# Kernel tuning notes

Measured on AMD Instinct MI355X. Metric: run time of the kernel, lower is better.

## Reference

```python
import jax, jax.numpy as jnp
import numpy as np

COMMITMENT_COST = 0.25
NUM_EMBEDDINGS = 512
EMBEDDING_DIM = 64


def setup_inputs() -> dict:
    key = jax.random.key(0)
    k1, k2 = jax.random.split(key)
    inputs = jax.random.normal(k1, (32, EMBEDDING_DIM, 64, 64), dtype=jnp.float32)  # NCHW
    embedding_weight = jax.random.normal(k2, (NUM_EMBEDDINGS, EMBEDDING_DIM), dtype=jnp.float32)
    return {"inputs": inputs, "embedding_weight": embedding_weight}


def reference(inputs, embedding_weight):
    # NCHW -> NHWC, flatten to [N, D]
    x = jnp.transpose(inputs, (0, 2, 3, 1))  # [B,H,W,D]
    input_shape = x.shape
    flat = x.reshape(-1, EMBEDDING_DIM)  # [N, D]

    distances = (jnp.sum(flat * flat, axis=1, keepdims=True)
                 + jnp.sum(embedding_weight * embedding_weight, axis=1)
                 - 2.0 * jnp.matmul(flat, embedding_weight.T))

    encoding_indices = jnp.argmin(distances, axis=1)  # [N]
    encodings = jax.nn.one_hot(encoding_indices, NUM_EMBEDDINGS, dtype=jnp.float32)  # [N, K]

    # quantized lookup (== encodings @ embedding_weight)
    quantized = jnp.take(embedding_weight, encoding_indices, axis=0).reshape(input_shape)

    # commitment loss (eval path; EMA buffer updates are a training-time side effect)
    encoder_loss = jnp.mean((jax.lax.stop_gradient(quantized) - x) ** 2)
    loss = COMMITMENT_COST * encoder_loss

    # straight-through estimator
    quantized_st = x + jax.lax.stop_gradient(quantized - x)

    avg_probs = jnp.mean(encodings, axis=0)
    perplexity = jnp.exp(-jnp.sum(avg_probs * jnp.log(avg_probs + 1e-10)))

    return (loss, jnp.transpose(quantized_st, (0, 3, 1, 2)), perplexity, encodings)
```

## Files before the change

### kernel.cpp

```cpp
#include <hip/hip_runtime.h>
#include <math.h>

#define N_ROWS 131072
#define D 64
#define K 512
#define BLK 512
#define ROWS_PER_BLK 512
#define GRID (N_ROWS / ROWS_PER_BLK)
#define MARGIN 4e-3f


typedef __attribute__((ext_vector_type(8))) _Float16 f16x8;
typedef __attribute__((ext_vector_type(4))) float    f32x4;

#define MFMA(a, b, c) __builtin_amdgcn_mfma_f32_16x16x32_f16((a), (b), (c), 0, 0, 0)

#define OFF_EH   0
#define OFF_EL   65536
#define OFF_XH   0
#define OFF_XL   65536
#define OFF_E2   131072
#define OFF_IDX  133120
#define OFF_REF  135168
#define ARENA_SZ 137216

__global__ __launch_bounds__(256) void vq_e2_kernel(
    const float* __restrict__ emb, float* __restrict__ e2)
{
    int k = blockIdx.x * blockDim.x + threadIdx.x;
    if (k < K) {
        const float* e = emb + k * D;
        float s = 0.f;
        #pragma unroll
        for (int d = 0; d < D; ++d) s = fmaf(e[d], e[d], s);
        e2[k] = s;
    }
}

__device__ __forceinline__ unsigned pk2(_Float16 a, _Float16 b) {
    return (unsigned)__builtin_bit_cast(unsigned short, a) |
           ((unsigned)__builtin_bit_cast(unsigned short, b) << 16);
}

#define CT_ALL(M) M(0) M(1) M(2) M(3)
#define UPD(rt, s, ki) { \
    bool lt1 = (s) < s1_##rt; bool lt2 = (s) < s2_##rt; \
    s2_##rt = lt1 ? s1_##rt : (lt2 ? (s) : s2_##rt); \
    i2_##rt = lt1 ? i1_##rt : (lt2 ? (ki) : i2_##rt); \
    s1_##rt = lt1 ? (s) : s1_##rt; \
    i1_##rt = lt1 ? (ki) : i1_##rt; }

__device__ __forceinline__ void dist_pass(
    const char* ebase, const float* e2L, int fq, int fr,
    f16x8 xh0_0, f16x8 xh0_1, f16x8 xl0_0, f16x8 xl0_1,
    f16x8 xh1_0, f16x8 xh1_1, f16x8 xl1_0, f16x8 xl1_1,
    int* s_idxL, int* s_refL, int row0)
{
    float s1_0 = INFINITY, s2_0 = INFINITY, s1_1 = INFINITY, s2_1 = INFINITY;
    int   i1_0 = 0, i2_0 = 0, i1_1 = 0, i2_1 = 0;

    for (int cb = 0; cb < 8; ++cb) {
        const int cbBase = cb * 64 + fq * 4;

#define LDE2(ct) f32x4 e2q##ct = *(const f32x4*)(e2L + cb * 64 + ct * 16 + fq * 4);
        CT_ALL(LDE2)
#undef LDE2

#define LDE(ct) \
        const int c##ct = cb * 64 + ct * 16 + fr; \
        const char* rb##ct = ebase + c##ct * 128; \
        const unsigned xr##ct = (unsigned)((c##ct & 7) << 4); \
        f16x8 eh##ct##_0 = *(const f16x8*)(rb##ct + OFF_EH + (((unsigned)(fq*16 +  0)) ^ xr##ct)); \
        f16x8 eh##ct##_1 = *(const f16x8*)(rb##ct + OFF_EH + (((unsigned)(fq*16 + 64)) ^ xr##ct)); \
        f16x8 el##ct##_0 = *(const f16x8*)(rb##ct + OFF_EL + (((unsigned)(fq*16 +  0)) ^ xr##ct)); \
        f16x8 el##ct##_1 = *(const f16x8*)(rb##ct + OFF_EL + (((unsigned)(fq*16 + 64)) ^ xr##ct));
        CT_ALL(LDE)
#undef LDE

#define ACC1(rt, ct) \
        f32x4 a##rt##_##ct = {0.f, 0.f, 0.f, 0.f}; \
        a##rt##_##ct = MFMA(eh##ct##_0, xh##rt##_0, a##rt##_##ct); \
        a##rt##_##ct = MFMA(eh##ct##_1, xh##rt##_1, a##rt##_##ct); \
        a##rt##_##ct = MFMA(el##ct##_0, xh##rt##_0, a##rt##_##ct); \
        a##rt##_##ct = MFMA(el##ct##_1, xh##rt##_1, a##rt##_##ct); \
        a##rt##_##ct = MFMA(eh##ct##_0, xl##rt##_0, a##rt##_##ct); \
        a##rt##_##ct = MFMA(eh##ct##_1, xl##rt##_1, a##rt##_##ct);
#define ACC_CT(ct) ACC1(0, ct) ACC1(1, ct)
        CT_ALL(ACC_CT)
#undef ACC_CT
#undef ACC1

#define SCJ(rt, ct, j) { \
        float s = fmaf(-2.f, a##rt##_##ct[j], e2q##ct[j]); \
        int ki = cbBase + ct * 16 + j; \
        UPD(rt, s, ki) }
#define SC4(rt, ct) SCJ(rt, ct, 0) SCJ(rt, ct, 1) SCJ(rt, ct, 2) SCJ(rt, ct, 3)
#define SC_CT(ct) SC4(0, ct) SC4(1, ct)
        CT_ALL(SC_CT)
#undef SC_CT
#undef SC4
#undef SCJ
    }

#define MERGE(rt, off) { \
    float b1 = __shfl_xor(s1_##rt, off); int bi1 = __shfl_xor(i1_##rt, off); \
    float b2 = __shfl_xor(s2_##rt, off); int bi2 = __shfl_xor(i2_##rt, off); \
    bool bf = (b1 < s1_##rt) || (b1 == s1_##rt && bi1 < i1_##rt); \
    float c1 = bf ? b1 : s1_##rt; int ci1 = bf ? bi1 : i1_##rt; \
    float lw = bf ? s1_##rt : b1; int lwi = bf ? i1_##rt : bi1; \
    float d2 = bf ? b2 : s2_##rt; int di2 = bf ? bi2 : i2_##rt; \
    bool ds = (d2 < lw) || (d2 == lw && di2 < lwi); \
    s1_##rt = c1; i1_##rt = ci1; \
    s2_##rt = ds ? d2 : lw; i2_##rt = ds ? di2 : lwi; }
    MERGE(0, 16) MERGE(0, 32) MERGE(1, 16) MERGE(1, 32)
#undef MERGE

    if (fq == 0) {
        s_idxL[row0 + fr] = i1_0;
        s_refL[row0 + fr] = (s2_0 - s1_0 < MARGIN) ? i2_0 : -1;
        s_idxL[row0 + fr + 16] = i1_1;
        s_refL[row0 + fr + 16] = (s2_1 - s1_1 < MARGIN) ? i2_1 : -1;
    }
}

__global__ __launch_bounds__(BLK, 2) void vq_dist_kernel(
    const float* __restrict__ in,
    const float* __restrict__ emb,
    const float* __restrict__ e2g,
    float* __restrict__ enc_out)
{
    __shared__ __align__(16) char s_arena[ARENA_SZ];
    float* e2L    = (float*)(s_arena + OFF_E2);
    int*   s_idxL = (int*)(s_arena + OFF_IDX);
    int*   s_refL = (int*)(s_arena + OFF_REF);

    const int tid  = threadIdx.x;
    const int lane = tid & 63;
    const int w    = tid >> 6;
    const int fr   = lane & 15;
    const int fq   = lane >> 4;

    {
        const int nn = blockIdx.x * ROWS_PER_BLK + tid;
        const int bb = nn >> 12, hww = nn & 4095;
        const float* xp = in + (size_t)bb * 262144 + hww;
        char* xhW = s_arena + OFF_XH;
        char* xlW = s_arena + OFF_XL;
        const unsigned rbase = (unsigned)tid * 128u;
        const unsigned rxor  = (unsigned)((tid & 7) << 4);
        #pragma unroll
        for (int i = 0; i < 64; i += 2) {
            float f0 = xp[i * 4096];
            float f1 = xp[(i + 1) * 4096];
            _Float16 h0 = (_Float16)f0; _Float16 l0 = (_Float16)(f0 - (float)h0);
            _Float16 h1 = (_Float16)f1; _Float16 l1 = (_Float16)(f1 - (float)h1);
            unsigned off = rbase + (((unsigned)(i * 2)) ^ rxor);
            *(unsigned*)(xhW + off) = pk2(h0, h1);
            *(unsigned*)(xlW + off) = pk2(l0, l1);
        }
    }
    __syncthreads();

    const char* xb = s_arena;
    const int xr0 = w * 64 + fr;
#define LDX1(t, half) \
    *(const f16x8*)(xb + OFF_XH + (unsigned)(xr0 + t * 16) * 128u + \
        (((unsigned)(fq * 16 + half * 64)) ^ ((unsigned)(((xr0 + t * 16) & 7) << 4))))
#define LDX1L(t, half) \
    *(const f16x8*)(xb + OFF_XL + (unsigned)(xr0 + t * 16) * 128u + \
        (((unsigned)(fq * 16 + half * 64)) ^ ((unsigned)(((xr0 + t * 16) & 7) << 4))))
#define LDXF(t) \
    f16x8 xh##t##_0 = LDX1(t, 0); \
    f16x8 xh##t##_1 = LDX1(t, 1); \
    f16x8 xl##t##_0 = LDX1L(t, 0); \
    f16x8 xl##t##_1 = LDX1L(t, 1);
    LDXF(0) LDXF(1) LDXF(2) LDXF(3)
#undef LDXF
#undef LDX1
#undef LDX1L
    __syncthreads();

    {
        char* eb = s_arena;
        #pragma unroll
        for (int it = 0; it < 16; ++it) {
            int j = tid + it * 512;
            int c = j >> 4, q = j & 15;
            float4 e = ((const float4*)emb)[j];
            _Float16 h0 = (_Float16)e.x; _Float16 l0 = (_Float16)(e.x - (float)h0);
            _Float16 h1 = (_Float16)e.y; _Float16 l1 = (_Float16)(e.y - (float)h1);
            _Float16 h2 = (_Float16)e.z; _Float16 l2 = (_Float16)(e.z - (float)h2);
            _Float16 h3 = (_Float16)e.w; _Float16 l3 = (_Float16)(e.w - (float)h3);
            unsigned xr = (unsigned)((c & 7) << 4);
            unsigned base = (unsigned)(c * 128) + (((unsigned)(q * 8)) ^ xr);
            *(uint2*)(eb + OFF_EH + base) = make_uint2(pk2(h0, h1), pk2(h2, h3));
            *(uint2*)(eb + OFF_EL + base) = make_uint2(pk2(l0, l1), pk2(l2, l3));
        }
        e2L[tid] = e2g[tid];
    }
    __syncthreads();

    dist_pass(s_arena, e2L, fq, fr,
              xh0_0, xh0_1, xl0_0, xl0_1, xh1_0, xh1_1, xl1_0, xl1_1,
              s_idxL, s_refL, w * 64);
    dist_pass(s_arena, e2L, fq, fr,
              xh2_0, xh2_1, xl2_0, xl2_1, xh3_0, xh3_1, xl3_0, xl3_1,
              s_idxL, s_refL, w * 64 + 32);

    {
        const int n = blockIdx.x * ROWS_PER_BLK + tid;
        int i1 = s_idxL[tid];
        int ir = s_refL[tid];
        *(int*)(enc_out + (size_t)n * K) = i1 | ((ir + 1) << 16);
    }
}

__global__ __launch_bounds__(256) void vq_out_kernel(
    const float* __restrict__ in,
    const float* __restrict__ emb,
    unsigned int* __restrict__ counts,
    unsigned long long* __restrict__ loss_acc,
    float* __restrict__ quant_out,
    float* __restrict__ enc)
{
    __shared__ unsigned int s_hist[K];
    __shared__ double s_red[256];
    const int tid = threadIdx.x;
    const int n = blockIdx.x * 256 + tid;
    s_hist[tid] = 0u; s_hist[tid + 256] = 0u;
    __syncthreads();

    const int b = n >> 12, hw = n & 4095;
    const float* xin = in + (size_t)b * 262144 + hw;
    const int packed = *(const int*)(enc + (size_t)n * K);
    int i1 = packed & 0xFFFF;
    const int ir = (packed >> 16) - 1;
    if (ir >= 0) {
        double dA = 0.0, dB = 0.0;
        const float* eA = emb + i1 * D;
        const float* eB = emb + ir * D;
        for (int d = 0; d < D; ++d) {
            double xv = (double)xin[d * 4096];
            double tA = xv - (double)eA[d]; dA = fma(tA, tA, dA);
            double tB = xv - (double)eB[d]; dB = fma(tB, tB, dB);
        }
        if (dB < dA || (dB == dA && ir < i1)) i1 = ir;
    }
    *(int*)(enc + (size_t)n * K) = i1;
    atomicAdd(&s_hist[i1], 1u);

    const float4* eq = (const float4*)(emb + (size_t)i1 * D);
    float* qout = quant_out + (size_t)b * 262144 + hw;
    float lsum = 0.f;
    #pragma unroll
    for (int i = 0; i < 16; ++i) {
        float4 q = eq[i];
        float x0 = xin[(4 * i + 0) * 4096], x1 = xin[(4 * i + 1) * 4096];
        float x2 = xin[(4 * i + 2) * 4096], x3 = xin[(4 * i + 3) * 4096];
        float d0 = q.x - x0; lsum = fmaf(d0, d0, lsum);
        float d1 = q.y - x1; lsum = fmaf(d1, d1, lsum);
        float d2 = q.z - x2; lsum = fmaf(d2, d2, lsum);
        float d3 = q.w - x3; lsum = fmaf(d3, d3, lsum);
        __builtin_nontemporal_store(q.x, &qout[(4 * i + 0) * 4096]);
        __builtin_nontemporal_store(q.y, &qout[(4 * i + 1) * 4096]);
        __builtin_nontemporal_store(q.z, &qout[(4 * i + 2) * 4096]);
        __builtin_nontemporal_store(q.w, &qout[(4 * i + 3) * 4096]);
    }

    s_red[tid] = (double)lsum;
    __syncthreads();
    for (int s = 128; s > 0; s >>= 1) {
        if (tid < s) s_red[tid] += s_red[tid + s];
        __syncthreads();
    }
    if (tid == 0) {
        unsigned long long q =
            (unsigned long long)(long long)llrint(s_red[0] * 1073741824.0);
        atomicAdd(loss_acc, q);
    }
    {
        unsigned int c0 = s_hist[tid];
        if (c0) atomicAdd(&counts[tid], c0);
        unsigned int c1 = s_hist[tid + 256];
        if (c1) atomicAdd(&counts[tid + 256], c1);
    }
}

__global__ __launch_bounds__(256) void vq_enc_kernel(float* __restrict__ enc)
{
    const int tid  = threadIdx.x;
    const int wv   = tid >> 6;
    const int lane = tid & 63;
    const size_t row0 = (size_t)blockIdx.x * 64 + (size_t)wv * 16;

    int idxs[16];
    #pragma unroll
    for (int i = 0; i < 16; ++i)
        idxs[i] = *(const int*)(enc + (row0 + i) * K);

    const int c0 = lane * 4;
    #pragma unroll
    for (int i = 0; i < 16; ++i) {
        const int idx = idxs[i];
        float* rp = enc + (row0 + i) * K;
        f32x4 v0, v1;
        v0.x = (c0 + 0 == idx) ? 1.f : 0.f;
        v0.y = (c0 + 1 == idx) ? 1.f : 0.f;
        v0.z = (c0 + 2 == idx) ? 1.f : 0.f;
        v0.w = (c0 + 3 == idx) ? 1.f : 0.f;
        v1.x = (256 + c0 + 0 == idx) ? 1.f : 0.f;
        v1.y = (256 + c0 + 1 == idx) ? 1.f : 0.f;
        v1.z = (256 + c0 + 2 == idx) ? 1.f : 0.f;
        v1.w = (256 + c0 + 3 == idx) ? 1.f : 0.f;
        __builtin_nontemporal_store(v0, (f32x4*)(rp + c0));
        __builtin_nontemporal_store(v1, (f32x4*)(rp + 256 + c0));
    }
}

__global__ __launch_bounds__(512) void vq_final_kernel(
    const unsigned int* __restrict__ counts,
    const unsigned long long* __restrict__ loss_acc,
    float* __restrict__ out_loss,
    float* __restrict__ out_perp)
{
    __shared__ double sp[512];
    int t = threadIdx.x;
    double p = (double)counts[t] / (double)N_ROWS;
    sp[t] = p * log(p + 1e-10);
    __syncthreads();
    for (int s = 256; s > 0; s >>= 1) {
        if (t < s) sp[t] += sp[t + s];
        __syncthreads();
    }
    if (t == 0) {
        double ls = (double)(long long)(*loss_acc) * (1.0 / 1073741824.0);
        *out_loss = (float)(0.25 * ls / 8388608.0);
        *out_perp = (float)exp(-sp[0]);
    }
}

extern "C" void kernel_launch(void* const* d_in, const int* in_sizes, int n_in,
                              void* d_out, int out_size, void* d_ws, size_t ws_size,
                              hipStream_t stream) {
    const float* in  = (const float*)d_in[0];
    const float* emb = (const float*)d_in[1];
    float* out = (float*)d_out;

    unsigned int* counts = (unsigned int*)d_ws;
    unsigned long long* loss_acc = (unsigned long long*)((char*)d_ws + 2048);
    float* e2 = (float*)((char*)d_ws + 4096);

    hipMemsetAsync(d_ws, 0, 2056, stream);
    vq_e2_kernel<<<2, 256, 0, stream>>>(emb, e2);
    vq_dist_kernel<<<GRID, BLK, 0, stream>>>(in, emb, e2, out + 8388610);
    vq_out_kernel<<<N_ROWS / 256, 256, 0, stream>>>(in, emb, counts, loss_acc,
                                                    out + 1, out + 8388610);
    vq_enc_kernel<<<N_ROWS / 64, 256, 0, stream>>>(out + 8388610);
    vq_final_kernel<<<1, 512, 0, stream>>>(counts, loss_acc, out, out + 8388609);
}
```

Before: 129.7 us.

## Fuse codebook-norm computation into dist kernel and one-hot write into output kernel

Removes the separate codebook squared-norm kernel by computing each norm inside the distance kernel with a lane-shuffle reduction while the codebook is staged to LDS. It also removes the separate one-hot encoding kernel: the output kernel keeps the final indices in shared memory and writes the one-hot rows itself. This saves two launches and the re-read of packed indices from global memory. The cost is that each dist block recomputes the norms, and the output kernel does more store work per block.

```diff
diff --git a/kernel.cpp b/kernel.cpp
--- a/kernel.cpp
+++ b/kernel.cpp
@@ -23,19 +23,6 @@
 #define OFF_IDX  133120
 #define OFF_REF  135168
 #define ARENA_SZ 137216
-
-__global__ __launch_bounds__(256) void vq_e2_kernel(
-    const float* __restrict__ emb, float* __restrict__ e2)
-{
-    int k = blockIdx.x * blockDim.x + threadIdx.x;
-    if (k < K) {
-        const float* e = emb + k * D;
-        float s = 0.f;
-        #pragma unroll
-        for (int d = 0; d < D; ++d) s = fmaf(e[d], e[d], s);
-        e2[k] = s;
-    }
-}
 
 __device__ __forceinline__ unsigned pk2(_Float16 a, _Float16 b) {
     return (unsigned)__builtin_bit_cast(unsigned short, a) |
@@ -126,7 +113,6 @@
 __global__ __launch_bounds__(BLK, 2) void vq_dist_kernel(
     const float* __restrict__ in,
     const float* __restrict__ emb,
-    const float* __restrict__ e2g,
     float* __restrict__ enc_out)
 {
     __shared__ __align__(16) char s_arena[ARENA_SZ];
@@ -195,8 +181,17 @@
             unsigned base = (unsigned)(c * 128) + (((unsigned)(q * 8)) ^ xr);
             *(uint2*)(eb + OFF_EH + base) = make_uint2(pk2(h0, h1), pk2(h2, h3));
             *(uint2*)(eb + OFF_EL + base) = make_uint2(pk2(l0, l1), pk2(l2, l3));
+
+            float p = e.x * e.x;
+            p = fmaf(e.y, e.y, p);
+            p = fmaf(e.z, e.z, p);
+            p = fmaf(e.w, e.w, p);
+            p += __shfl_xor(p, 1);
+            p += __shfl_xor(p, 2);
+            p += __shfl_xor(p, 4);
+            p += __shfl_xor(p, 8);
+            if (q == 0) e2L[c] = p;
         }
-        e2L[tid] = e2g[tid];
     }
     __syncthreads();
 
@@ -224,6 +219,7 @@
     float* __restrict__ enc)
 {
     __shared__ unsigned int s_hist[K];
+    __shared__ int s_idx[256];
     __shared__ double s_red[256];
     const int tid = threadIdx.x;
     const int n = blockIdx.x * 256 + tid;
@@ -246,7 +242,7 @@
         }
         if (dB < dA || (dB == dA && ir < i1)) i1 = ir;
     }
-    *(int*)(enc + (size_t)n * K) = i1;
+    s_idx[tid] = i1;
     atomicAdd(&s_hist[i1], 1u);
 
     const float4* eq = (const float4*)(emb + (size_t)i1 * D);
@@ -266,8 +262,33 @@
         __builtin_nontemporal_store(q.z, &qout[(4 * i + 2) * 4096]);
         __builtin_nontemporal_store(q.w, &qout[(4 * i + 3) * 4096]);
     }
-
     s_red[tid] = (double)lsum;
+    __syncthreads();
+
+    {
+        const int wv   = tid >> 6;
+        const int lane = tid & 63;
+        const int r0   = wv * 64;
+        float* brow = enc + ((size_t)blockIdx.x * 256 + r0) * K;
+        const int c0 = lane * 4;
+        #pragma unroll 8
+        for (int i = 0; i < 64; ++i) {
+            const int idx = s_idx[r0 + i];
+            float* rp = brow + (size_t)i * K;
+            f32x4 v0, v1;
+            v0.x = (c0 + 0 == idx) ? 1.f : 0.f;
+            v0.y = (c0 + 1 == idx) ? 1.f : 0.f;
+            v0.z = (c0 + 2 == idx) ? 1.f : 0.f;
+            v0.w = (c0 + 3 == idx) ? 1.f : 0.f;
+            v1.x = (256 + c0 + 0 == idx) ? 1.f : 0.f;
+            v1.y = (256 + c0 + 1 == idx) ? 1.f : 0.f;
+            v1.z = (256 + c0 + 2 == idx) ? 1.f : 0.f;
+            v1.w = (256 + c0 + 3 == idx) ? 1.f : 0.f;
+            __builtin_nontemporal_store(v0, (f32x4*)(rp + c0));
+            __builtin_nontemporal_store(v1, (f32x4*)(rp + 256 + c0));
+        }
+    }
+
     __syncthreads();
     for (int s = 128; s > 0; s >>= 1) {
         if (tid < s) s_red[tid] += s_red[tid + s];
@@ -279,41 +300,10 @@
         atomicAdd(loss_acc, q);
     }
     {
-        unsigned int c0 = s_hist[tid];
-        if (c0) atomicAdd(&counts[tid], c0);
-        unsigned int c1 = s_hist[tid + 256];
-        if (c1) atomicAdd(&counts[tid + 256], c1);
-    }
-}
-
-__global__ __launch_bounds__(256) void vq_enc_kernel(float* __restrict__ enc)
-{
-    const int tid  = threadIdx.x;
-    const int wv   = tid >> 6;
-    const int lane = tid & 63;
-    const size_t row0 = (size_t)blockIdx.x * 64 + (size_t)wv * 16;
-
-    int idxs[16];
-    #pragma unroll
-    for (int i = 0; i < 16; ++i)
-        idxs[i] = *(const int*)(enc + (row0 + i) * K);
-
-    const int c0 = lane * 4;
-    #pragma unroll
-    for (int i = 0; i < 16; ++i) {
-        const int idx = idxs[i];
-        float* rp = enc + (row0 + i) * K;
-        f32x4 v0, v1;
-        v0.x = (c0 + 0 == idx) ? 1.f : 0.f;
-        v0.y = (c0 + 1 == idx) ? 1.f : 0.f;
-        v0.z = (c0 + 2 == idx) ? 1.f : 0.f;
-        v0.w = (c0 + 3 == idx) ? 1.f : 0.f;
-        v1.x = (256 + c0 + 0 == idx) ? 1.f : 0.f;
-        v1.y = (256 + c0 + 1 == idx) ? 1.f : 0.f;
-        v1.z = (256 + c0 + 2 == idx) ? 1.f : 0.f;
-        v1.w = (256 + c0 + 3 == idx) ? 1.f : 0.f;
-        __builtin_nontemporal_store(v0, (f32x4*)(rp + c0));
-        __builtin_nontemporal_store(v1, (f32x4*)(rp + 256 + c0));
+        unsigned int c0h = s_hist[tid];
+        if (c0h) atomicAdd(&counts[tid], c0h);
+        unsigned int c1h = s_hist[tid + 256];
+        if (c1h) atomicAdd(&counts[tid + 256], c1h);
     }
 }
 
@@ -348,13 +338,10 @@
 
     unsigned int* counts = (unsigned int*)d_ws;
     unsigned long long* loss_acc = (unsigned long long*)((char*)d_ws + 2048);
-    float* e2 = (float*)((char*)d_ws + 4096);
 
     hipMemsetAsync(d_ws, 0, 2056, stream);
-    vq_e2_kernel<<<2, 256, 0, stream>>>(emb, e2);
-    vq_dist_kernel<<<GRID, BLK, 0, stream>>>(in, emb, e2, out + 8388610);
+    vq_dist_kernel<<<GRID, BLK, 0, stream>>>(in, emb, out + 8388610);
     vq_out_kernel<<<N_ROWS / 256, 256, 0, stream>>>(in, emb, counts, loss_acc,
                                                     out + 1, out + 8388610);
-    vq_enc_kernel<<<N_ROWS / 64, 256, 0, stream>>>(out + 8388610);
     vq_final_kernel<<<1, 512, 0, stream>>>(counts, loss_acc, out, out + 8388609);
 }
```

Result: slower. 135.4 us (+4.5%).
